# Performance work log

Measured on AMD Instinct MI355X. Metric: run time of the kernel, lower is better.

Reference implementation:

```python
import jax, jax.numpy as jnp
import numpy as np

N_NODES = 100000
N_EDGES = 1600000
IN_DIM = 128
HID = 64


def _init_linear(key, fan_in, fan_out):
    kw, kb = jax.random.split(key)
    bound = 1.0 / np.sqrt(fan_in)
    W = jax.random.uniform(kw, (fan_in, fan_out), jnp.float32, -bound, bound)
    b = jax.random.uniform(kb, (fan_out,), jnp.float32, -bound, bound)
    return W, b


def setup_inputs() -> dict:
    key = jax.random.key(0)
    ks = jax.random.split(key, 6)
    x = jax.random.normal(ks[0], (N_NODES, IN_DIM), jnp.float32)
    edge_index = jax.random.randint(ks[1], (2, N_EDGES), 0, N_NODES, jnp.int64)
    W_pre, b_pre = _init_linear(ks[2], IN_DIM, HID)
    W1, b1 = _init_linear(ks[3], HID, HID)
    W2, b2 = _init_linear(ks[4], HID, HID)
    W3, b3 = _init_linear(ks[5], HID, HID)
    return {"x": x, "edge_index": edge_index, "W_pre": W_pre, "b_pre": b_pre,
            "W1": W1, "b1": b1, "W2": W2, "b2": b2, "W3": W3, "b3": b3}


def _gcn_layer(h, src, dst, dinv, W, b):
    # PyG GCNConv: h' = D^{-1/2} (A + I) D^{-1/2} (h W) + b, deg from A+I
    n = h.shape[0]
    hw = h @ W                                  # [N, out]
    norm = dinv[src] * dinv[dst]                # [E]
    msg = hw[src] * norm[:, None]               # gather + scale  [E, out]
    agg = jax.ops.segment_sum(msg, dst, num_segments=n)  # scatter-add
    agg = agg + hw * (dinv * dinv)[:, None]     # self-loop term (norm = dinv_i^2)
    return agg + b


def reference(x, edge_index, W_pre, b_pre, W1, b1, W2, b2, W3, b3):
    src, dst = edge_index[0], edge_index[1]
    n = x.shape[0]
    # degree of A + I (self loops added, as in GCNConv default)
    deg = jax.ops.segment_sum(jnp.ones(src.shape[0], x.dtype), dst, num_segments=n) + 1.0
    dinv = jax.lax.rsqrt(deg)

    h = x @ W_pre + b_pre                       # feature_pre linear
    h = jax.nn.relu(_gcn_layer(h, src, dst, dinv, W1, b1))  # dropout is identity in eval
    h = jax.nn.relu(_gcn_layer(h, src, dst, dinv, W2, b2))
    h = _gcn_layer(h, src, dst, dinv, W3, b3)
    # F.normalize(p=2, dim=-1) with eps=1e-12
    nrm = jnp.linalg.norm(h, axis=-1, keepdims=True)
    return h / jnp.maximum(nrm, 1e-12)
```

## Files before the change

### kernel.cpp

```cpp
#include <hip/hip_runtime.h>

#define N_NODES 100000
#define N_EDGES 1600000
#define IN_DIM 128
#define HID 64
#define NB 782
#define NT64 1563
#define NGROUP 25000

typedef __attribute__((ext_vector_type(8))) _Float16 h8v;
typedef __attribute__((ext_vector_type(4))) float f4v;

struct Args {
  const float* x; const int* ei;
  const float* Wp; const float* bp;
  const float* W1; const float* b1;
  const float* W2; const float* b2;
  const float* W3; const float* b3;
  float* out;
  _Float16* bufA16; _Float16* hw16;
  int* pairs; int* csr; int* offs; float* dinv;
  int* bsz; int* bboff; int* bcur;
  _Float16* WpH; _Float16* WpL; _Float16* W1H; _Float16* W1L;
  _Float16* W2H; _Float16* W2L; _Float16* W3H; _Float16* W3L;
};

__device__ __forceinline__ void d_split(const float* __restrict__ W,
                                        _Float16* __restrict__ hi,
                                        _Float16* __restrict__ lo, int K, int i) {
  int k = i >> 6, n = i & 63;
  float v = W[i];
  _Float16 h = (_Float16)v;
  float r = v - (float)h;
  hi[n * K + k] = h;
  lo[n * K + k] = (_Float16)r;
}

__global__ __launch_bounds__(256) void f_prep(Args a) {
  int blk = blockIdx.x, t = threadIdx.x;
  if (blk < 32) d_split(a.Wp, a.WpH, a.WpL, IN_DIM, blk * 256 + t);
  else if (blk < 48) d_split(a.W1, a.W1H, a.W1L, HID, (blk - 32) * 256 + t);
  else if (blk < 64) d_split(a.W2, a.W2H, a.W2L, HID, (blk - 48) * 256 + t);
  else d_split(a.W3, a.W3H, a.W3L, HID, (blk - 64) * 256 + t);
}

__global__ __launch_bounds__(256) void f_bhist(Args a) {
  __shared__ int cnt[NB];
  int t = threadIdx.x;
  for (int i = t; i < NB; i += 256) cnt[i] = 0;
  __syncthreads();
  int e0 = blockIdx.x * 8192, e1 = min(e0 + 8192, N_EDGES);
  for (int e = e0 + t; e < e1; e += 256)
    atomicAdd(&cnt[a.ei[N_EDGES + e] >> 7], 1);
  __syncthreads();
  for (int i = t; i < NB; i += 256)
    if (cnt[i]) atomicAdd(&a.bsz[i], cnt[i]);
}

__global__ __launch_bounds__(256) void f_bscan(Args a) {
  __shared__ int sm[256];
  int t = threadIdx.x;
  int c[4];
  int idx0 = t * 4;
#pragma unroll
  for (int j = 0; j < 4; ++j) c[j] = (idx0 + j < NB) ? a.bsz[idx0 + j] : 0;
  int tsum = c[0] + c[1] + c[2] + c[3];
  int val = tsum;
  sm[t] = val;
  __syncthreads();
  for (int off = 1; off < 256; off <<= 1) {
    int u = (t >= off) ? sm[t - off] : 0;
    __syncthreads();
    val += u;
    sm[t] = val;
    __syncthreads();
  }
  int excl = val - tsum;
#pragma unroll
  for (int j = 0; j < 4; ++j) {
    int idx = idx0 + j;
    if (idx < NB) { a.bboff[idx] = excl; a.bcur[idx] = excl; }
    excl += c[j];
  }
  if (t == 255) a.bboff[NB] = val;
}

__global__ __launch_bounds__(256) void f_partition(Args a) {
  __shared__ int cnt[NB];
  __shared__ int base[NB];
  int t = threadIdx.x;
  for (int i = t; i < NB; i += 256) cnt[i] = 0;
  __syncthreads();
  int e0 = blockIdx.x * 8192, e1 = min(e0 + 8192, N_EDGES);
  for (int e = e0 + t; e < e1; e += 256)
    atomicAdd(&cnt[a.ei[N_EDGES + e] >> 7], 1);
  __syncthreads();
  for (int i = t; i < NB; i += 256) {
    int c = cnt[i];
    base[i] = c ? atomicAdd(&a.bcur[i], c) : 0;
    cnt[i] = 0;
  }
  __syncthreads();
  for (int e = e0 + t; e < e1; e += 256) {
    int s = a.ei[e];
    int d = a.ei[N_EDGES + e];
    int b = d >> 7;
    int r = atomicAdd(&cnt[b], 1);
    a.pairs[base[b] + r] = ((d & 127) << 17) | s;
  }
}

__global__ __launch_bounds__(256) void f_csrdeg(Args a) {
  __shared__ int ldeg[128];
  __shared__ int sc[128];
  __shared__ int lcur[128];
  int t = threadIdx.x;
  int b = blockIdx.x;
  int node0 = b << 7;
  int nloc = min(128, N_NODES - node0);
  int beg = a.bboff[b], end = a.bboff[b + 1];
  if (t < 128) ldeg[t] = 0;
  __syncthreads();
  for (int i = beg + t; i < end; i += 256)
    atomicAdd(&ldeg[(a.pairs[i] >> 17) & 127], 1);
  __syncthreads();
  int dv = (t < 128) ? ldeg[t] : 0;
  if (t < 128) sc[t] = dv;
  __syncthreads();
  for (int off = 1; off < 128; off <<= 1) {
    int u = (t >= off && t < 128) ? sc[t - off] : 0;
    __syncthreads();
    if (t < 128) sc[t] += u;
    __syncthreads();
  }
  if (t < nloc) {
    int o = beg + sc[t] - dv;
    a.offs[node0 + t] = o;
    lcur[t] = o;
    a.dinv[node0 + t] = rsqrtf((float)dv + 1.0f);
  }
  if (b == NB - 1 && t == 0) a.offs[N_NODES] = N_EDGES;
  __syncthreads();
  for (int i = beg + t; i < end; i += 256) {
    int p = a.pairs[i];
    int pos = atomicAdd(&lcur[(p >> 17) & 127], 1);
    a.csr[pos] = p & 131071;
  }
}

__global__ __launch_bounds__(256) void f_gemm_pre(Args a) {
  const int K = IN_DIM;
  int wave = threadIdx.x >> 6;
  int lane = threadIdx.x & 63;
  int fi = lane & 15;
  int quad = lane >> 4;
  int r0 = blockIdx.x * 64 + wave * 16;
  int row_l = r0 + fi;
  if (row_l >= N_NODES) row_l = N_NODES - 1;
  const float* xp = a.x + (size_t)row_l * K + quad * 8;

  f4v acc[4];
#pragma unroll
  for (int ct = 0; ct < 4; ++ct) acc[ct] = (f4v){0.f, 0.f, 0.f, 0.f};

#pragma unroll
  for (int k0 = 0; k0 < K; k0 += 32) {
    f4v xa = *(const f4v*)(xp + k0);
    f4v xb = *(const f4v*)(xp + k0 + 4);
    h8v ah, al;
#pragma unroll
    for (int j = 0; j < 4; ++j) {
      _Float16 h = (_Float16)xa[j];
      ah[j] = h;
      al[j] = (_Float16)(xa[j] - (float)h);
    }
#pragma unroll
    for (int j = 0; j < 4; ++j) {
      _Float16 h = (_Float16)xb[j];
      ah[4 + j] = h;
      al[4 + j] = (_Float16)(xb[j] - (float)h);
    }
    const _Float16* whp = a.WpH + (size_t)fi * K + k0 + quad * 8;
    const _Float16* wlp = a.WpL + (size_t)fi * K + k0 + quad * 8;
#pragma unroll
    for (int ct = 0; ct < 4; ++ct) {
      h8v bh = *(const h8v*)(whp + (size_t)ct * 16 * K);
      h8v bl = *(const h8v*)(wlp + (size_t)ct * 16 * K);
      acc[ct] = __builtin_amdgcn_mfma_f32_16x16x32_f16(ah, bh, acc[ct], 0, 0, 0);
      acc[ct] = __builtin_amdgcn_mfma_f32_16x16x32_f16(al, bh, acc[ct], 0, 0, 0);
      acc[ct] = __builtin_amdgcn_mfma_f32_16x16x32_f16(ah, bl, acc[ct], 0, 0, 0);
    }
  }
#pragma unroll
  for (int ct = 0; ct < 4; ++ct) {
    float bv = a.bp[ct * 16 + fi];
#pragma unroll
    for (int j = 0; j < 4; ++j) {
      int orow = r0 + quad * 4 + j;
      if (orow < N_NODES)
        a.bufA16[(size_t)orow * HID + ct * 16 + fi] = (_Float16)(acc[ct][j] + bv);
    }
  }
}

__global__ __launch_bounds__(256) void f_gemm64(Args a, const _Float16* __restrict__ Wh,
                                                const _Float16* __restrict__ Wl) {
  const int K = HID;
  int wave = threadIdx.x >> 6;
  int lane = threadIdx.x & 63;
  int fi = lane & 15;
  int quad = lane >> 4;
  int r0 = blockIdx.x * 64 + wave * 16;
  int row_l = r0 + fi;
  if (row_l >= N_NODES) row_l = N_NODES - 1;
  const _Float16* xp = a.bufA16 + (size_t)row_l * K + quad * 8;

  f4v acc[4];
#pragma unroll
  for (int ct = 0; ct < 4; ++ct) acc[ct] = (f4v){0.f, 0.f, 0.f, 0.f};

#pragma unroll
  for (int k0 = 0; k0 < K; k0 += 32) {
    h8v av = *(const h8v*)(xp + k0);
    const _Float16* whp = Wh + (size_t)fi * K + k0 + quad * 8;
    const _Float16* wlp = Wl + (size_t)fi * K + k0 + quad * 8;
#pragma unroll
    for (int ct = 0; ct < 4; ++ct) {
      h8v bh = *(const h8v*)(whp + (size_t)ct * 16 * K);
      h8v bl = *(const h8v*)(wlp + (size_t)ct * 16 * K);
      acc[ct] = __builtin_amdgcn_mfma_f32_16x16x32_f16(av, bh, acc[ct], 0, 0, 0);
      acc[ct] = __builtin_amdgcn_mfma_f32_16x16x32_f16(av, bl, acc[ct], 0, 0, 0);
    }
  }
#pragma unroll
  for (int ct = 0; ct < 4; ++ct) {
#pragma unroll
    for (int j = 0; j < 4; ++j) {
      int orow = r0 + quad * 4 + j;
      if (orow < N_NODES)
        a.hw16[(size_t)orow * HID + ct * 16 + fi] = (_Float16)acc[ct][j];
    }
  }
}

template <int MODE>
__device__ __forceinline__ void d_agg(int grp, const _Float16* __restrict__ hw,
                                      const int* __restrict__ offs,
                                      const int* __restrict__ csr,
                                      const float* __restrict__ dinv,
                                      const float* __restrict__ bias,
                                      _Float16* __restrict__ out16,
                                      float* __restrict__ out32) {
  int node = grp * 4 + (threadIdx.x >> 6);
  int lane = threadIdx.x & 63;
  int oct = lane >> 3;
  int fi = lane & 7;
  float di = dinv[node];
  int beg = offs[node];
  int end = offs[node + 1];

  float acc[8];
#pragma unroll
  for (int c = 0; c < 8; ++c) acc[c] = 0.f;

  if (oct == 0) {
    h8v hv = *(const h8v*)(hw + (size_t)node * HID + fi * 8);
    float w = di * di;
#pragma unroll
    for (int c = 0; c < 8; ++c) acc[c] += (float)hv[c] * w;
  }
  for (int e0 = beg + oct; e0 < end; e0 += 32) {
    int ss[4];
    float ww[4];
#pragma unroll
    for (int j = 0; j < 4; ++j) {
      int e = e0 + 8 * j;
      bool v = e < end;
      int s = csr[v ? e : beg];
      ss[j] = v ? s : node;
      ww[j] = v ? di : 0.0f;
    }
#pragma unroll
    for (int j = 0; j < 4; ++j) ww[j] *= dinv[ss[j]];
    h8v hv[4];
#pragma unroll
    for (int j = 0; j < 4; ++j)
      hv[j] = *(const h8v*)(hw + (size_t)ss[j] * HID + fi * 8);
#pragma unroll
    for (int j = 0; j < 4; ++j)
#pragma unroll
      for (int c = 0; c < 8; ++c) acc[c] += (float)hv[j][c] * ww[j];
  }
#pragma unroll
  for (int c = 0; c < 8; ++c) {
    float v = acc[c];
    v += __shfl_xor(v, 8);
    v += __shfl_xor(v, 16);
    v += __shfl_xor(v, 32);
    acc[c] = v;
  }
  if (oct == 0) {
#pragma unroll
    for (int c = 0; c < 8; ++c) acc[c] += bias[fi * 8 + c];
    if (MODE == 0) {
      h8v o;
#pragma unroll
      for (int c = 0; c < 8; ++c) o[c] = (_Float16)fmaxf(acc[c], 0.f);
      *(h8v*)(out16 + (size_t)node * HID + fi * 8) = o;
    } else {
      float ss = 0.f;
#pragma unroll
      for (int c = 0; c < 8; ++c) ss += acc[c] * acc[c];
      ss += __shfl_xor(ss, 1);
      ss += __shfl_xor(ss, 2);
      ss += __shfl_xor(ss, 4);
      float sc = 1.0f / fmaxf(sqrtf(ss), 1e-12f);
      f4v o0 = {acc[0] * sc, acc[1] * sc, acc[2] * sc, acc[3] * sc};
      f4v o1 = {acc[4] * sc, acc[5] * sc, acc[6] * sc, acc[7] * sc};
      *(f4v*)(out32 + (size_t)node * HID + fi * 8) = o0;
      *(f4v*)(out32 + (size_t)node * HID + fi * 8 + 4) = o1;
    }
  }
}

__global__ __launch_bounds__(256) void f_agg_relu(Args a, const float* bias) {
  d_agg<0>(blockIdx.x, a.hw16, a.offs, a.csr, a.dinv, bias, a.bufA16, nullptr);
}

__global__ __launch_bounds__(256) void f_agg_norm(Args a) {
  d_agg<1>(blockIdx.x, a.hw16, a.offs, a.csr, a.dinv, a.b3, nullptr, a.out);
}

extern "C" void kernel_launch(void* const* d_in, const int* in_sizes, int n_in,
                              void* d_out, int out_size, void* d_ws, size_t ws_size,
                              hipStream_t stream) {
  char* ws = (char*)d_ws;
  Args a;
  a.x  = (const float*)d_in[0];
  a.ei = (const int*)d_in[1];
  a.Wp = (const float*)d_in[2];  a.bp = (const float*)d_in[3];
  a.W1 = (const float*)d_in[4];  a.b1 = (const float*)d_in[5];
  a.W2 = (const float*)d_in[6];  a.b2 = (const float*)d_in[7];
  a.W3 = (const float*)d_in[8];  a.b3 = (const float*)d_in[9];
  a.out  = (float*)d_out;
  a.bufA16 = (_Float16*)(ws + 0);
  a.hw16   = (_Float16*)(ws + 12800000);
  a.pairs  = (int*)(ws + 25600000);
  a.csr    = (int*)(ws + 32000000);
  a.offs   = (int*)(ws + 38400000);
  a.dinv   = (float*)(ws + 38800016);
  a.bsz    = (int*)(ws + 39200016);
  a.bboff  = (int*)(ws + 39203152);
  a.bcur   = (int*)(ws + 39206288);
  a.WpH = (_Float16*)(ws + 39210000);
  a.WpL = (_Float16*)(ws + 39226384);
  a.W1H = (_Float16*)(ws + 39242768);
  a.W1L = (_Float16*)(ws + 39250960);
  a.W2H = (_Float16*)(ws + 39259152);
  a.W2L = (_Float16*)(ws + 39267344);
  a.W3H = (_Float16*)(ws + 39275536);
  a.W3L = (_Float16*)(ws + 39283728);

  (void)hipMemsetAsync(a.bsz, 0, NB * sizeof(int), stream);
  f_prep<<<80, 256, 0, stream>>>(a);
  f_bhist<<<196, 256, 0, stream>>>(a);
  f_bscan<<<1, 256, 0, stream>>>(a);
  f_partition<<<196, 256, 0, stream>>>(a);
  f_csrdeg<<<NB, 256, 0, stream>>>(a);
  f_gemm_pre<<<NT64, 256, 0, stream>>>(a);
  f_gemm64<<<NT64, 256, 0, stream>>>(a, a.W1H, a.W1L);
  f_agg_relu<<<NGROUP, 256, 0, stream>>>(a, a.b1);
  f_gemm64<<<NT64, 256, 0, stream>>>(a, a.W2H, a.W2L);
  f_agg_relu<<<NGROUP, 256, 0, stream>>>(a, a.b2);
  f_gemm64<<<NT64, 256, 0, stream>>>(a, a.W3H, a.W3L);
  f_agg_norm<<<NGROUP, 256, 0, stream>>>(a);
}
```

Measured before the change: 382.5 us.

## Fold dinv scaling into GEMM output and pad zero row for edge tails

The hidden GEMMs now write hw pre-scaled by dinv of the source row. The aggregation then sums raw fp16 neighbor rows and multiplies by the destination dinv once at the end, which removes the per-edge dinv gather and multiply. Invalid tail edges point to a zero row appended at index N_NODES, and four gathered vectors are summed in fp16 before conversion to fp32. GEMM blocks now cover 16 rows with one 16-column tile per wave, and the partition and histogram kernels use smaller edge chunks with more blocks. The fp16 partial sums reduce accuracy, and the workspace layout shifts to make room for the padded row.

```diff
diff --git a/kernel.cpp b/kernel.cpp
--- a/kernel.cpp
+++ b/kernel.cpp
@@ -5,8 +5,9 @@
 #define IN_DIM 128
 #define HID 64
 #define NB 782
-#define NT64 1563
+#define NGEMM 6250
 #define NGROUP 25000
+#define PART_BLOCKS 391
 
 typedef __attribute__((ext_vector_type(8))) _Float16 h8v;
 typedef __attribute__((ext_vector_type(4))) float f4v;
@@ -41,7 +42,8 @@
   if (blk < 32) d_split(a.Wp, a.WpH, a.WpL, IN_DIM, blk * 256 + t);
   else if (blk < 48) d_split(a.W1, a.W1H, a.W1L, HID, (blk - 32) * 256 + t);
   else if (blk < 64) d_split(a.W2, a.W2H, a.W2L, HID, (blk - 48) * 256 + t);
-  else d_split(a.W3, a.W3H, a.W3L, HID, (blk - 64) * 256 + t);
+  else if (blk < 80) d_split(a.W3, a.W3H, a.W3L, HID, (blk - 64) * 256 + t);
+  else if (t < HID) a.hw16[(size_t)N_NODES * HID + t] = (_Float16)0.f;
 }
 
 __global__ __launch_bounds__(256) void f_bhist(Args a) {
@@ -49,7 +51,7 @@
   int t = threadIdx.x;
   for (int i = t; i < NB; i += 256) cnt[i] = 0;
   __syncthreads();
-  int e0 = blockIdx.x * 8192, e1 = min(e0 + 8192, N_EDGES);
+  int e0 = blockIdx.x * 4096, e1 = min(e0 + 4096, N_EDGES);
   for (int e = e0 + t; e < e1; e += 256)
     atomicAdd(&cnt[a.ei[N_EDGES + e] >> 7], 1);
   __syncthreads();
@@ -91,7 +93,7 @@
   int t = threadIdx.x;
   for (int i = t; i < NB; i += 256) cnt[i] = 0;
   __syncthreads();
-  int e0 = blockIdx.x * 8192, e1 = min(e0 + 8192, N_EDGES);
+  int e0 = blockIdx.x * 4096, e1 = min(e0 + 4096, N_EDGES);
   for (int e = e0 + t; e < e1; e += 256)
     atomicAdd(&cnt[a.ei[N_EDGES + e] >> 7], 1);
   __syncthreads();
@@ -150,19 +152,14 @@
 
 __global__ __launch_bounds__(256) void f_gemm_pre(Args a) {
   const int K = IN_DIM;
-  int wave = threadIdx.x >> 6;
+  int w = threadIdx.x >> 6;
   int lane = threadIdx.x & 63;
   int fi = lane & 15;
   int quad = lane >> 4;
-  int r0 = blockIdx.x * 64 + wave * 16;
-  int row_l = r0 + fi;
-  if (row_l >= N_NODES) row_l = N_NODES - 1;
-  const float* xp = a.x + (size_t)row_l * K + quad * 8;
-
-  f4v acc[4];
-#pragma unroll
-  for (int ct = 0; ct < 4; ++ct) acc[ct] = (f4v){0.f, 0.f, 0.f, 0.f};
-
+  int r0 = blockIdx.x * 16;
+  const float* xp = a.x + (size_t)(r0 + fi) * K + quad * 8;
+
+  f4v acc = {0.f, 0.f, 0.f, 0.f};
 #pragma unroll
   for (int k0 = 0; k0 < K; k0 += 32) {
     f4v xa = *(const f4v*)(xp + k0);
@@ -180,66 +177,47 @@
       ah[4 + j] = h;
       al[4 + j] = (_Float16)(xb[j] - (float)h);
     }
-    const _Float16* whp = a.WpH + (size_t)fi * K + k0 + quad * 8;
-    const _Float16* wlp = a.WpL + (size_t)fi * K + k0 + quad * 8;
-#pragma unroll
-    for (int ct = 0; ct < 4; ++ct) {
-      h8v bh = *(const h8v*)(whp + (size_t)ct * 16 * K);
-      h8v bl = *(const h8v*)(wlp + (size_t)ct * 16 * K);
-      acc[ct] = __builtin_amdgcn_mfma_f32_16x16x32_f16(ah, bh, acc[ct], 0, 0, 0);
-      acc[ct] = __builtin_amdgcn_mfma_f32_16x16x32_f16(al, bh, acc[ct], 0, 0, 0);
-      acc[ct] = __builtin_amdgcn_mfma_f32_16x16x32_f16(ah, bl, acc[ct], 0, 0, 0);
-    }
-  }
-#pragma unroll
-  for (int ct = 0; ct < 4; ++ct) {
-    float bv = a.bp[ct * 16 + fi];
-#pragma unroll
-    for (int j = 0; j < 4; ++j) {
-      int orow = r0 + quad * 4 + j;
-      if (orow < N_NODES)
-        a.bufA16[(size_t)orow * HID + ct * 16 + fi] = (_Float16)(acc[ct][j] + bv);
-    }
+    const _Float16* whp = a.WpH + (size_t)(w * 16 + fi) * K + k0 + quad * 8;
+    const _Float16* wlp = a.WpL + (size_t)(w * 16 + fi) * K + k0 + quad * 8;
+    h8v bh = *(const h8v*)whp;
+    h8v bl = *(const h8v*)wlp;
+    acc = __builtin_amdgcn_mfma_f32_16x16x32_f16(ah, bh, acc, 0, 0, 0);
+    acc = __builtin_amdgcn_mfma_f32_16x16x32_f16(al, bh, acc, 0, 0, 0);
+    acc = __builtin_amdgcn_mfma_f32_16x16x32_f16(ah, bl, acc, 0, 0, 0);
+  }
+  float bv = a.bp[w * 16 + fi];
+#pragma unroll
+  for (int j = 0; j < 4; ++j) {
+    int orow = r0 + quad * 4 + j;
+    a.bufA16[(size_t)orow * HID + w * 16 + fi] = (_Float16)(acc[j] + bv);
   }
 }
 
 __global__ __launch_bounds__(256) void f_gemm64(Args a, const _Float16* __restrict__ Wh,
                                                 const _Float16* __restrict__ Wl) {
   const int K = HID;
-  int wave = threadIdx.x >> 6;
+  int w = threadIdx.x >> 6;
   int lane = threadIdx.x & 63;
   int fi = lane & 15;
   int quad = lane >> 4;
-  int r0 = blockIdx.x * 64 + wave * 16;
-  int row_l = r0 + fi;
-  if (row_l >= N_NODES) row_l = N_NODES - 1;
-  const _Float16* xp = a.bufA16 + (size_t)row_l * K + quad * 8;
-
-  f4v acc[4];
-#pragma unroll
-  for (int ct = 0; ct < 4; ++ct) acc[ct] = (f4v){0.f, 0.f, 0.f, 0.f};
-
+  int r0 = blockIdx.x * 16;
+  const _Float16* xp = a.bufA16 + (size_t)(r0 + fi) * K + quad * 8;
+
+  f4v acc = {0.f, 0.f, 0.f, 0.f};
 #pragma unroll
   for (int k0 = 0; k0 < K; k0 += 32) {
     h8v av = *(const h8v*)(xp + k0);
-    const _Float16* whp = Wh + (size_t)fi * K + k0 + quad * 8;
-    const _Float16* wlp = Wl + (size_t)fi * K + k0 + quad * 8;
-#pragma unroll
-    for (int ct = 0; ct < 4; ++ct) {
-      h8v bh = *(const h8v*)(whp + (size_t)ct * 16 * K);
-      h8v bl = *(const h8v*)(wlp + (size_t)ct * 16 * K);
-      acc[ct] = __builtin_amdgcn_mfma_f32_16x16x32_f16(av, bh, acc[ct], 0, 0, 0);
-      acc[ct] = __builtin_amdgcn_mfma_f32_16x16x32_f16(av, bl, acc[ct], 0, 0, 0);
-    }
-  }
-#pragma unroll
-  for (int ct = 0; ct < 4; ++ct) {
-#pragma unroll
-    for (int j = 0; j < 4; ++j) {
-      int orow = r0 + quad * 4 + j;
-      if (orow < N_NODES)
-        a.hw16[(size_t)orow * HID + ct * 16 + fi] = (_Float16)acc[ct][j];
-    }
+    const _Float16* whp = Wh + (size_t)(w * 16 + fi) * K + k0 + quad * 8;
+    const _Float16* wlp = Wl + (size_t)(w * 16 + fi) * K + k0 + quad * 8;
+    h8v bh = *(const h8v*)whp;
+    h8v bl = *(const h8v*)wlp;
+    acc = __builtin_amdgcn_mfma_f32_16x16x32_f16(av, bh, acc, 0, 0, 0);
+    acc = __builtin_amdgcn_mfma_f32_16x16x32_f16(av, bl, acc, 0, 0, 0);
+  }
+#pragma unroll
+  for (int j = 0; j < 4; ++j) {
+    int orow = r0 + quad * 4 + j;
+    a.hw16[(size_t)orow * HID + w * 16 + fi] = (_Float16)(acc[j] * a.dinv[orow]);
   }
 }
 
@@ -265,31 +243,24 @@
 
   if (oct == 0) {
     h8v hv = *(const h8v*)(hw + (size_t)node * HID + fi * 8);
-    float w = di * di;
-#pragma unroll
-    for (int c = 0; c < 8; ++c) acc[c] += (float)hv[c] * w;
+#pragma unroll
+    for (int c = 0; c < 8; ++c) acc[c] += (float)hv[c];
   }
   for (int e0 = beg + oct; e0 < end; e0 += 32) {
     int ss[4];
-    float ww[4];
 #pragma unroll
     for (int j = 0; j < 4; ++j) {
       int e = e0 + 8 * j;
-      bool v = e < end;
-      int s = csr[v ? e : beg];
-      ss[j] = v ? s : node;
-      ww[j] = v ? di : 0.0f;
+      int s = csr[min(e, end - 1)];
+      ss[j] = (e < end) ? s : N_NODES;
     }
-#pragma unroll
-    for (int j = 0; j < 4; ++j) ww[j] *= dinv[ss[j]];
     h8v hv[4];
 #pragma unroll
     for (int j = 0; j < 4; ++j)
       hv[j] = *(const h8v*)(hw + (size_t)ss[j] * HID + fi * 8);
-#pragma unroll
-    for (int j = 0; j < 4; ++j)
-#pragma unroll
-      for (int c = 0; c < 8; ++c) acc[c] += (float)hv[j][c] * ww[j];
+    h8v hs = (hv[0] + hv[1]) + (hv[2] + hv[3]);
+#pragma unroll
+    for (int c = 0; c < 8; ++c) acc[c] += (float)hs[c];
   }
 #pragma unroll
   for (int c = 0; c < 8; ++c) {
@@ -301,7 +272,7 @@
   }
   if (oct == 0) {
 #pragma unroll
-    for (int c = 0; c < 8; ++c) acc[c] += bias[fi * 8 + c];
+    for (int c = 0; c < 8; ++c) acc[c] = acc[c] * di + bias[fi * 8 + c];
     if (MODE == 0) {
       h8v o;
 #pragma unroll
@@ -345,33 +316,33 @@
   a.out  = (float*)d_out;
   a.bufA16 = (_Float16*)(ws + 0);
   a.hw16   = (_Float16*)(ws + 12800000);
-  a.pairs  = (int*)(ws + 25600000);
-  a.csr    = (int*)(ws + 32000000);
-  a.offs   = (int*)(ws + 38400000);
-  a.dinv   = (float*)(ws + 38800016);
-  a.bsz    = (int*)(ws + 39200016);
-  a.bboff  = (int*)(ws + 39203152);
-  a.bcur   = (int*)(ws + 39206288);
-  a.WpH = (_Float16*)(ws + 39210000);
-  a.WpL = (_Float16*)(ws + 39226384);
-  a.W1H = (_Float16*)(ws + 39242768);
-  a.W1L = (_Float16*)(ws + 39250960);
-  a.W2H = (_Float16*)(ws + 39259152);
-  a.W2L = (_Float16*)(ws + 39267344);
-  a.W3H = (_Float16*)(ws + 39275536);
-  a.W3L = (_Float16*)(ws + 39283728);
+  a.pairs  = (int*)(ws + 25600256);
+  a.csr    = (int*)(ws + 32000256);
+  a.offs   = (int*)(ws + 38400256);
+  a.dinv   = (float*)(ws + 38800264);
+  a.bsz    = (int*)(ws + 39200264);
+  a.bboff  = (int*)(ws + 39203400);
+  a.bcur   = (int*)(ws + 39206536);
+  a.WpH = (_Float16*)(ws + 39209672);
+  a.WpL = (_Float16*)(ws + 39226056);
+  a.W1H = (_Float16*)(ws + 39242440);
+  a.W1L = (_Float16*)(ws + 39250632);
+  a.W2H = (_Float16*)(ws + 39258824);
+  a.W2L = (_Float16*)(ws + 39267016);
+  a.W3H = (_Float16*)(ws + 39275208);
+  a.W3L = (_Float16*)(ws + 39283400);
 
   (void)hipMemsetAsync(a.bsz, 0, NB * sizeof(int), stream);
-  f_prep<<<80, 256, 0, stream>>>(a);
-  f_bhist<<<196, 256, 0, stream>>>(a);
+  f_prep<<<81, 256, 0, stream>>>(a);
+  f_bhist<<<PART_BLOCKS, 256, 0, stream>>>(a);
   f_bscan<<<1, 256, 0, stream>>>(a);
-  f_partition<<<196, 256, 0, stream>>>(a);
+  f_partition<<<PART_BLOCKS, 256, 0, stream>>>(a);
   f_csrdeg<<<NB, 256, 0, stream>>>(a);
-  f_gemm_pre<<<NT64, 256, 0, stream>>>(a);
-  f_gemm64<<<NT64, 256, 0, stream>>>(a, a.W1H, a.W1L);
+  f_gemm_pre<<<NGEMM, 256, 0, stream>>>(a);
+  f_gemm64<<<NGEMM, 256, 0, stream>>>(a, a.W1H, a.W1L);
   f_agg_relu<<<NGROUP, 256, 0, stream>>>(a, a.b1);
-  f_gemm64<<<NT64, 256, 0, stream>>>(a, a.W2H, a.W2L);
+  f_gemm64<<<NGEMM, 256, 0, stream>>>(a, a.W2H, a.W2L);
   f_agg_relu<<<NGROUP, 256, 0, stream>>>(a, a.b2);
-  f_gemm64<<<NT64, 256, 0, stream>>>(a, a.W3H, a.W3L);
+  f_gemm64<<<NGEMM, 256, 0, stream>>>(a, a.W3H, a.W3L);
   f_agg_norm<<<NGROUP, 256, 0, stream>>>(a);
 }
```

New measurement: 397.6 us. +4.0%, slower.
